# Kernel tuning notes

Measured on AMD Instinct MI355X. Metric: run time of the kernel, lower is better.

Reference implementation:

```python
import jax, jax.numpy as jnp
import numpy as np

Vx, Vy, B, N, C, H, M_VIEWS = 8, 8, 4, 196, 768, 12, 4
DH = C // H
SCALE = DH ** -0.5
HID = 4 * C


def _layer_norm(x, w, b, eps=1e-5):
    mu = jnp.mean(x, axis=-1, keepdims=True)
    var = jnp.mean((x - mu) ** 2, axis=-1, keepdims=True)
    return (x - mu) / jnp.sqrt(var + eps) * w + b


def setup_inputs() -> dict:
    key = jax.random.key(0)
    ks = jax.random.split(key, 32)
    s = 0.02
    inp = {
        "xs": jax.random.normal(ks[0], (Vx, B, N, C), jnp.float32),
        "ys": jax.random.normal(ks[1], (Vy, B, N, C), jnp.float32),
        "xposes": jax.random.randint(ks[2], (Vx, B, N, 2), 0, N),
        "yposes": jax.random.randint(ks[3], (Vy, B, N, 2), 0, N),
        "rel_ids": jax.random.randint(ks[4], (Vx * M_VIEWS,), 0, Vy),
        "M": M_VIEWS,
        # self-attention params (qkv_bias=False, proj has bias)
        "qkv_w": jax.random.normal(ks[5], (3 * C, C), jnp.float32) * s,
        "attn_proj_w": jax.random.normal(ks[6], (C, C), jnp.float32) * s,
        "attn_proj_b": jnp.zeros((C,), jnp.float32),
        # cross-attention params
        "q_w": jax.random.normal(ks[7], (C, C), jnp.float32) * s,
        "k_w": jax.random.normal(ks[8], (C, C), jnp.float32) * s,
        "v_w": jax.random.normal(ks[9], (C, C), jnp.float32) * s,
        "cross_proj_w": jax.random.normal(ks[10], (C, C), jnp.float32) * s,
        "cross_proj_b": jnp.zeros((C,), jnp.float32),
        # MLP
        "fc1_w": jax.random.normal(ks[11], (HID, C), jnp.float32) * s,
        "fc1_b": jnp.zeros((HID,), jnp.float32),
        "fc2_w": jax.random.normal(ks[12], (C, HID), jnp.float32) * s,
        "fc2_b": jnp.zeros((C,), jnp.float32),
        # layer norms
        "ln1_w": jnp.ones((C,), jnp.float32), "ln1_b": jnp.zeros((C,), jnp.float32),
        "ln2_w": jnp.ones((C,), jnp.float32), "ln2_b": jnp.zeros((C,), jnp.float32),
        "ln3_w": jnp.ones((C,), jnp.float32), "ln3_b": jnp.zeros((C,), jnp.float32),
        "lny_w": jnp.ones((C,), jnp.float32), "lny_b": jnp.zeros((C,), jnp.float32),
    }
    return inp


def _forward(xs, ys, rel_ids, M,
             qkv_w, attn_proj_w, attn_proj_b,
             q_w, k_w, v_w, cross_proj_w, cross_proj_b,
             fc1_w, fc1_b, fc2_w, fc2_b,
             ln1_w, ln1_b, ln2_w, ln2_b, ln3_w, ln3_b, lny_w, lny_b):
    vx, b, nx, c = xs.shape
    vy, _, ny, _ = ys.shape
    x = xs.reshape(vx * b, nx, c)

    # ---- self-attention over each target view (rope=None) ----
    h = _layer_norm(x, ln1_w, ln1_b)
    qkv = (h @ qkv_w.T).reshape(vx * b, nx, 3, H, DH)
    q = jnp.transpose(qkv[:, :, 0], (0, 2, 1, 3))  # (VB,H,N,dh)
    k = jnp.transpose(qkv[:, :, 1], (0, 2, 1, 3))
    v = jnp.transpose(qkv[:, :, 2], (0, 2, 1, 3))
    attn = jax.nn.softmax(jnp.einsum('bhnd,bhkd->bhnk', q, k) * SCALE, axis=-1)
    o = jnp.einsum('bhnk,bhkd->bnhd', attn, v).reshape(vx * b, nx, c)
    x = x + (o @ attn_proj_w.T + attn_proj_b)

    # ---- batched multi-view cross-attention ----
    xn = _layer_norm(x.reshape(vx, b, nx, c), ln2_w, ln2_b)
    yn = _layer_norm(ys, lny_w, lny_b)
    qs = (xn @ q_w.T).reshape(vx, b, nx, H, DH)
    ks = (yn @ k_w.T).reshape(vy, b, ny, H, DH)
    vs = (yn @ v_w.T).reshape(vy, b, ny, H, DH)
    ks_r = ks[rel_ids].reshape(vx, M, b, ny, H, DH)  # index_select + group
    vs_r = vs[rel_ids].reshape(vx, M, b, ny, H, DH)
    # q is broadcast across the M group dim (no materialized expand)
    scores = jnp.einsum('vbnhd,vmbkhd->vmbhnk', qs, ks_r) * SCALE
    a = jax.nn.softmax(scores, axis=-1)
    o = jnp.einsum('vmbhnk,vmbkhd->vmbnhd', a, vs_r).reshape(vx, M, b, nx, c)
    o = o @ cross_proj_w.T + cross_proj_b  # (Vx,M,B,Nx,C)
    merged = jnp.max(o, axis=1).reshape(vx * b, nx, c)  # max-merge over M
    x = x + merged

    # ---- MLP ----
    h = _layer_norm(x, ln3_w, ln3_b)
    x = x + (jax.nn.gelu(h @ fc1_w.T + fc1_b, approximate=False) @ fc2_w.T + fc2_b)
    return x.reshape(vx, b, nx, c)


def reference(xs, ys, xposes, yposes, rel_ids, M,
              qkv_w, attn_proj_w, attn_proj_b,
              q_w, k_w, v_w, cross_proj_w, cross_proj_b,
              fc1_w, fc1_b, fc2_w, fc2_b,
              ln1_w, ln1_b, ln2_w, ln2_b, ln3_w, ln3_b, lny_w, lny_b):
    # xposes/yposes unused because rope=None in this configuration
    return _forward(xs, ys, rel_ids, M,
                    qkv_w, attn_proj_w, attn_proj_b,
                    q_w, k_w, v_w, cross_proj_w, cross_proj_b,
                    fc1_w, fc1_b, fc2_w, fc2_b,
                    ln1_w, ln1_b, ln2_w, ln2_b, ln3_w, ln3_b, lny_w, lny_b)
```

## Files before the change

kernel.cpp:

```cpp
#include <hip/hip_runtime.h>
#include <hip/hip_bf16.h>
#include <stdint.h>
#include <math.h>

#define H_ 12
#define NQ 196
#define CD 768
#define HIDD 3072
#define VX 8
#define VY 8
#define BB 4
#define MV 4
#define VBB 32
#define ROWS 6272
#define CROSS_ROWS 25088
#define SCALE_LOG2E 0.180336880260608f

typedef __attribute__((ext_vector_type(8))) short short8;
typedef __attribute__((ext_vector_type(4))) float f32x4;
typedef __attribute__((ext_vector_type(4))) unsigned short u16x4;
typedef unsigned short u16;

#define AS1 __attribute__((address_space(1)))
#define AS3 __attribute__((address_space(3)))

__device__ __forceinline__ float bf2f(u16 u){
  union { unsigned int i; float f; } v; v.i = ((unsigned int)u) << 16; return v.f;
}
__device__ __forceinline__ u16 f2bf(float f){
  union { unsigned int i; float f; } v; v.f = f;
  return (u16)((v.i + 0x7fff + ((v.i >> 16) & 1)) >> 16);
}
__device__ __forceinline__ unsigned int f2u(float f){
  union { unsigned int i; float f; } v; v.f = f; return v.i;
}

struct CastSegs {
  const float* src[8];
  u16* dst[8];
  int cum[9];
};
__global__ __launch_bounds__(256) void k_cast_all(CastSegs segs){
  int i = blockIdx.x * 256 + threadIdx.x;
  if (i >= segs.cum[8]) return;
  int s = 0;
  #pragma unroll
  for (int k = 1; k < 8; k++) s += (i >= segs.cum[k]);
  const int off = i - segs.cum[s];
  segs.dst[s][off] = f2bf(segs.src[s][off]);
}

__device__ __forceinline__ void ln_row(const float* __restrict__ x,
    const float* __restrict__ w, const float* __restrict__ b,
    u16* __restrict__ out, int row, int tid){
  const float* xr = x + (size_t)row * CD;
  float v0 = xr[tid], v1 = xr[tid + 256], v2 = xr[tid + 512];
  float s  = v0 + v1 + v2;
  float s2 = v0*v0 + v1*v1 + v2*v2;
  __shared__ float red[8];
  const int lane = tid & 63, wid = tid >> 6;
  #pragma unroll
  for (int o = 32; o; o >>= 1){ s += __shfl_down(s, o); s2 += __shfl_down(s2, o); }
  if (lane == 0){ red[wid] = s; red[wid + 4] = s2; }
  __syncthreads();
  if (tid == 0){
    red[0] = red[0] + red[1] + red[2] + red[3];
    red[4] = red[4] + red[5] + red[6] + red[7];
  }
  __syncthreads();
  const float mu   = red[0] * (1.f/768.f);
  const float var  = red[4] * (1.f/768.f) - mu*mu;
  const float rstd = rsqrtf(var + 1e-5f);
  u16* orow = out + (size_t)row * CD;
  orow[tid]       = f2bf((v0 - mu)*rstd*w[tid]       + b[tid]);
  orow[tid + 256] = f2bf((v1 - mu)*rstd*w[tid + 256] + b[tid + 256]);
  orow[tid + 512] = f2bf((v2 - mu)*rstd*w[tid + 512] + b[tid + 512]);
}

__global__ __launch_bounds__(256) void k_ln_bf16(const float* __restrict__ x,
    const float* __restrict__ w, const float* __restrict__ b, u16* __restrict__ out){
  ln_row(x, w, b, out, blockIdx.x, threadIdx.x);
}

__global__ __launch_bounds__(256) void k_ln_bf16x2(
    const float* __restrict__ x0, const float* __restrict__ w0,
    const float* __restrict__ b0, u16* __restrict__ o0,
    const float* __restrict__ x1, const float* __restrict__ w1,
    const float* __restrict__ b1, u16* __restrict__ o1){
  const int bid = blockIdx.x;
  if (bid < ROWS) ln_row(x0, w0, b0, o0, bid, threadIdx.x);
  else            ln_row(x1, w1, b1, o1, bid - ROWS, threadIdx.x);
}

template<int EPI, int TM>
__global__ __launch_bounds__(256) void k_gemm_bt(
    const u16* __restrict__ A, const u16* __restrict__ B,
    float* __restrict__ Cf, u16* __restrict__ Cb,
    const float* __restrict__ bias, const float* __restrict__ resid,
    int M, int N, int K){
  __shared__ u16 As[TM * 64];
  __shared__ u16 Bs[128 * 64];
  const int tid  = threadIdx.x;
  const int lane = tid & 63;
  const int wave = tid >> 6;
  const int wr = wave >> 1, wc = wave & 1;

  const int gx = gridDim.x;
  const int nwg = gx * gridDim.y;
  const int orig = blockIdx.y * gx + blockIdx.x;
  const int q8 = nwg >> 3, r8 = nwg & 7;
  const int xcd = orig & 7, bse = orig >> 3;
  const int wg = (xcd < r8 ? xcd * (q8 + 1) : r8 * (q8 + 1) + (xcd - r8) * q8) + bse;
  const int m0 = (wg / gx) * TM, n0 = (wg % gx) * 128;

  constexpr int MF = TM / 64;
  f32x4 acc[TM/32][4];
  #pragma unroll
  for (int i = 0; i < TM/32; i++)
    #pragma unroll
    for (int j = 0; j < 4; j++) acc[i][j] = (f32x4){0.f, 0.f, 0.f, 0.f};
  (void)MF;

  const int lrow = lane >> 3;
  const int lcol = ((lane & 7) ^ lrow) * 8;
  const u16* arow = A + (size_t)(m0 + wave*(TM/4) + lrow) * K + lcol;
  const u16* brow = B + (size_t)(n0 + wave*32 + lrow) * K + lcol;

  for (int k0 = 0; k0 < K; k0 += 64){
    #pragma unroll
    for (int i = 0; i < TM/32; i++)
      __builtin_amdgcn_global_load_lds(
        (const AS1 void*)(arow + (size_t)i*8*K + k0),
        (AS3 void*)(As + (wave*(TM/4) + i*8)*64), 16, 0, 0);
    #pragma unroll
    for (int i = 0; i < 4; i++)
      __builtin_amdgcn_global_load_lds(
        (const AS1 void*)(brow + (size_t)i*8*K + k0),
        (AS3 void*)(Bs + (wave*32 + i*8)*64), 16, 0, 0);
    __syncthreads();
    const u16* ab = As + (wr*(TM/2) + (lane & 15))*64;
    const u16* bb = Bs + (wc*64 + (lane & 15))*64;
    const int r7 = lane & 7;
    #pragma unroll
    for (int kk = 0; kk < 2; kk++){
      const int sl = (((lane >> 4) + 4*kk) ^ r7) * 8;
      short8 af[TM/32], bfr[4];
      #pragma unroll
      for (int f = 0; f < TM/32; f++) af[f] = *(const short8*)(ab + f*1024 + sl);
      #pragma unroll
      for (int f = 0; f < 4; f++)     bfr[f] = *(const short8*)(bb + f*1024 + sl);
      #pragma unroll
      for (int i = 0; i < TM/32; i++)
        #pragma unroll
        for (int j = 0; j < 4; j++)
          acc[i][j] = __builtin_amdgcn_mfma_f32_16x16x32_bf16(af[i], bfr[j], acc[i][j], 0, 0, 0);
    }
    __syncthreads();
  }

  #pragma unroll
  for (int i = 0; i < TM/32; i++){
    const int rb = m0 + wr*(TM/2) + i*16 + (lane >> 4)*4;
    #pragma unroll
    for (int j = 0; j < 4; j++){
      const int col = n0 + wc*64 + j*16 + (lane & 15);
      #pragma unroll
      for (int r = 0; r < 4; r++){
        const size_t idx = (size_t)(rb + r) * N + col;
        const float v = acc[i][j][r];
        if (EPI == 0){
          Cb[idx] = f2bf(v);
        } else if (EPI == 1){
          Cf[idx] = v + bias[col] + resid[idx];
        } else if (EPI == 2){
          Cf[idx] = v + bias[col];
        } else if (EPI == 3){
          float g = v + bias[col];
          g = 0.5f * g * (1.f + erff(g * 0.70710678118654752f));
          Cb[idx] = f2bf(g);
        } else {
          Cb[idx] = f2bf(v + bias[col]);
        }
      }
    }
  }
}

template<int MODE>
__global__ __launch_bounds__(256) void k_attn_mfma(
    const u16* __restrict__ Qb, const u16* __restrict__ Kb, const u16* __restrict__ Vb,
    u16* __restrict__ Ob, const int* __restrict__ rel_ids){
  __shared__ u16 Kl[2][2048];
  __shared__ u16 Vl[2][2048];

  size_t qbase, kbase, vbase, obase;
  int qstr, kstr;
  if (MODE == 0){
    const int vb = blockIdx.x / H_, h = blockIdx.x % H_;
    qbase = (size_t)vb * NQ * 2304 + h * 64; qstr = 2304;
    kbase = qbase + 768; vbase = qbase + 1536; kstr = 2304;
    obase = (size_t)vb * NQ * CD + h * 64;
  } else {
    const int h = blockIdx.x % H_; int t = blockIdx.x / H_;
    const int b = t % BB; t /= BB;
    const int m = t % MV; const int vx = t / MV;
    const int rel = rel_ids[vx * MV + m];
    qbase = ((size_t)(vx * BB + b) * NQ) * CD + h * 64; qstr = CD;
    kbase = ((size_t)(rel * BB + b) * NQ) * 1536 + h * 64; kstr = 1536;
    vbase = kbase + 768;
    obase = ((size_t)((vx * MV + m) * BB + b) * NQ) * CD + h * 64;
  }

  const int tid  = threadIdx.x;
  const int lane = tid & 63;
  const int wave = tid >> 6;
  const int lq   = lane & 15;
  const int g    = lane >> 4;

  short8 qfrag[4][2];
  #pragma unroll
  for (int qf = 0; qf < 4; qf++){
    int qrow = wave*64 + qf*16 + lq; if (qrow > 195) qrow = 195;
    const u16* qp = Qb + qbase + (size_t)qrow * qstr + g*8;
    qfrag[qf][0] = *(const short8*)(qp);
    qfrag[qf][1] = *(const short8*)(qp + 32);
  }

  f32x4 oacc[4][4];
  #pragma unroll
  for (int i = 0; i < 4; i++)
    #pragma unroll
    for (int j = 0; j < 4; j++) oacc[i][j] = (f32x4){0.f,0.f,0.f,0.f};
  float l_[4] = {0.f, 0.f, 0.f, 0.f};

  const int skey  = tid >> 3;
  const int sslot = (tid & 7) ^ (skey & 7);
  const int vkey = lane >> 1;
  const int vdh  = wave*16 + (lane & 1)*8;

  auto STAGE = [&](int nb, int t0n){
    int kg = t0n + skey; if (kg > 195) kg = 195;
    __builtin_amdgcn_global_load_lds(
        (const AS1 void*)(Kb + kbase + (size_t)kg*kstr + sslot*8),
        (AS3 void*)(&Kl[nb][wave*512]), 16, 0, 0);
    int vg = t0n + vkey; if (vg > 195) vg = 195;
    __builtin_amdgcn_global_load_lds(
        (const AS1 void*)(Vb + vbase + (size_t)vg*kstr + vdh),
        (AS3 void*)(&Vl[nb][wave*512]), 16, 0, 0);
  };

  union U8 { unsigned u[4]; short8 s; };

  STAGE(0, 0);
  __syncthreads();

  for (int t = 0; t < 7; t++){
    const int cb = t & 1;
    const int t0 = t * 32;
    if (t < 6) STAGE(cb ^ 1, t0 + 32);

    f32x4 sacc[4][2];
    #pragma unroll
    for (int qf = 0; qf < 4; qf++)
      #pragma unroll
      for (int kf = 0; kf < 2; kf++) sacc[qf][kf] = (f32x4){0.f,0.f,0.f,0.f};
    __builtin_amdgcn_s_setprio(1);
    #pragma unroll
    for (int kf = 0; kf < 2; kf++){
      const int key = kf*16 + lq;
      #pragma unroll
      for (int ks = 0; ks < 2; ks++){
        short8 kfrag = *(const short8*)(&Kl[cb][key*64 + (((ks<<2) + g) ^ (key & 7))*8]);
        #pragma unroll
        for (int qf = 0; qf < 4; qf++)
          sacc[qf][kf] = __builtin_amdgcn_mfma_f32_16x16x32_bf16(kfrag, qfrag[qf][ks], sacc[qf][kf], 0, 0, 0);
      }
    }
    __builtin_amdgcn_s_setprio(0);

    const AS3 u16* vp = (const AS3 u16*)(&Vl[cb][0]) + (size_t)lane*4;
    uint2 tr0a, tr0b, tr1a, tr1b, tr2a, tr2b, tr3a, tr3b;
    asm volatile("ds_read_b64_tr_b16 %0, %1 offset:0"    : "=&v"(tr0a) : "v"(vp));
    asm volatile("ds_read_b64_tr_b16 %0, %1 offset:512"  : "=&v"(tr0b) : "v"(vp));
    asm volatile("ds_read_b64_tr_b16 %0, %1 offset:1024" : "=&v"(tr1a) : "v"(vp));
    asm volatile("ds_read_b64_tr_b16 %0, %1 offset:1536" : "=&v"(tr1b) : "v"(vp));
    asm volatile("ds_read_b64_tr_b16 %0, %1 offset:2048" : "=&v"(tr2a) : "v"(vp));
    asm volatile("ds_read_b64_tr_b16 %0, %1 offset:2560" : "=&v"(tr2b) : "v"(vp));
    asm volatile("ds_read_b64_tr_b16 %0, %1 offset:3072" : "=&v"(tr3a) : "v"(vp));
    asm volatile("ds_read_b64_tr_b16 %0, %1 offset:3584" : "=&v"(tr3b) : "v"(vp));

    short8 vfrag[4];
    #pragma unroll
    for (int qf = 0; qf < 4; qf++){
      float p[8], ps = 0.f;
      #pragma unroll
      for (int kf = 0; kf < 2; kf++)
        #pragma unroll
        for (int r = 0; r < 4; r++){
          const int key = t0 + kf*16 + g*4 + r;
          const float e = exp2f(sacc[qf][kf][r] * SCALE_LOG2E);
          p[kf*4 + r] = (key < 196) ? e : 0.f;
          ps += p[kf*4 + r];
        }
      ps += __shfl_xor(ps, 16);
      ps += __shfl_xor(ps, 32);
      l_[qf] += ps;
      U8 pk;
      pk.u[0] = (f2u(p[0]) >> 16) | (f2u(p[1]) & 0xffff0000u);
      pk.u[1] = (f2u(p[2]) >> 16) | (f2u(p[3]) & 0xffff0000u);
      pk.u[2] = (f2u(p[4]) >> 16) | (f2u(p[5]) & 0xffff0000u);
      pk.u[3] = (f2u(p[6]) >> 16) | (f2u(p[7]) & 0xffff0000u);

      if (qf == 0){
        asm volatile("s_waitcnt lgkmcnt(0)" ::: "memory");
        __builtin_amdgcn_sched_barrier(0);
        U8 v0; v0.u[0]=tr0a.x; v0.u[1]=tr0a.y; v0.u[2]=tr0b.x; v0.u[3]=tr0b.y; vfrag[0]=v0.s;
        U8 v1; v1.u[0]=tr1a.x; v1.u[1]=tr1a.y; v1.u[2]=tr1b.x; v1.u[3]=tr1b.y; vfrag[1]=v1.s;
        U8 v2; v2.u[0]=tr2a.x; v2.u[1]=tr2a.y; v2.u[2]=tr2b.x; v2.u[3]=tr2b.y; vfrag[2]=v2.s;
        U8 v3; v3.u[0]=tr3a.x; v3.u[1]=tr3a.y; v3.u[2]=tr3b.x; v3.u[3]=tr3b.y; vfrag[3]=v3.s;
      }
      __builtin_amdgcn_s_setprio(1);
      #pragma unroll
      for (int dhf = 0; dhf < 4; dhf++)
        oacc[qf][dhf] = __builtin_amdgcn_mfma_f32_16x16x32_bf16(vfrag[dhf], pk.s, oacc[qf][dhf], 0, 0, 0);
      __builtin_amdgcn_s_setprio(0);
    }
    __syncthreads();
  }

  #pragma unroll
  for (int qf = 0; qf < 4; qf++){
    const int qrow = wave*64 + qf*16 + lq;
    if (qrow < 196){
      const float inv = 1.f / l_[qf];
      u16* orow = Ob + obase + (size_t)qrow * CD;
      #pragma unroll
      for (int dhf = 0; dhf < 4; dhf++){
        uint2 pk;
        pk.x = (unsigned)f2bf(oacc[qf][dhf][0]*inv) | ((unsigned)f2bf(oacc[qf][dhf][1]*inv) << 16);
        pk.y = (unsigned)f2bf(oacc[qf][dhf][2]*inv) | ((unsigned)f2bf(oacc[qf][dhf][3]*inv) << 16);
        *(uint2*)(orow + dhf*16 + g*4) = pk;
      }
    }
  }
}

__global__ __launch_bounds__(256) void k_maxmerge(const u16* __restrict__ op,
                                                  float* __restrict__ x){
  const int idx = blockIdx.x * 256 + threadIdx.x;
  const int n4 = VX * BB * NQ * CD / 4;
  if (idx >= n4) return;
  const int inner = idx % (NQ * CD / 4);
  const int vb = idx / (NQ * CD / 4);
  const int vx = vb >> 2, b = vb & 3;
  const size_t ms = (size_t)BB * NQ * CD / 4;
  const size_t base = ((size_t)vx * MV * BB + b) * (NQ * CD / 4) + inner;
  const u16x4* op4 = (const u16x4*)op;
  u16x4 a0 = op4[base], a1 = op4[base + ms], a2 = op4[base + 2*ms], a3 = op4[base + 3*ms];
  float* xo = x + (size_t)idx * 4;
  #pragma unroll
  for (int j = 0; j < 4; j++){
    float v = fmaxf(fmaxf(bf2f(a0[j]), bf2f(a1[j])), fmaxf(bf2f(a2[j]), bf2f(a3[j])));
    xo[j] += v;
  }
}

extern "C" void kernel_launch(void* const* d_in, const int* in_sizes, int n_in,
                              void* d_out, int out_size, void* d_ws, size_t ws_size,
                              hipStream_t stream){
  const float* xs           = (const float*)d_in[0];
  const float* ys           = (const float*)d_in[1];
  const int*   rel_ids      = (const int*)  d_in[4];
  const float* qkv_w        = (const float*)d_in[6];
  const float* attn_proj_w  = (const float*)d_in[7];
  const float* attn_proj_b  = (const float*)d_in[8];
  const float* q_w          = (const float*)d_in[9];
  const float* k_w          = (const float*)d_in[10];
  const float* v_w          = (const float*)d_in[11];
  const float* cross_proj_w = (const float*)d_in[12];
  const float* cross_proj_b = (const float*)d_in[13];
  const float* fc1_w        = (const float*)d_in[14];
  const float* fc1_b        = (const float*)d_in[15];
  const float* fc2_w        = (const float*)d_in[16];
  const float* fc2_b        = (const float*)d_in[17];
  const float* ln1_w        = (const float*)d_in[18];
  const float* ln1_b        = (const float*)d_in[19];
  const float* ln2_w        = (const float*)d_in[20];
  const float* ln2_b        = (const float*)d_in[21];
  const float* ln3_w        = (const float*)d_in[22];
  const float* ln3_b        = (const float*)d_in[23];
  const float* lny_w        = (const float*)d_in[24];
  const float* lny_b        = (const float*)d_in[25];
  float* out = (float*)d_out;

  char* ws = (char*)d_ws;
  size_t off = 0;
  auto alloc = [&](size_t bytes) -> char* {
    char* p = ws + off; off += (bytes + 255) & ~(size_t)255; return p;
  };
  u16* wb_qkv   = (u16*)alloc((size_t)2304*768*2);
  u16* wb_aproj = (u16*)alloc((size_t)768*768*2);
  u16* wb_q     = (u16*)alloc((size_t)768*768*2);
  u16* wb_kv    = (u16*)alloc((size_t)1536*768*2);
  u16* wb_cproj = (u16*)alloc((size_t)768*768*2);
  u16* wb_fc1   = (u16*)alloc((size_t)3072*768*2);
  u16* wb_fc2   = (u16*)alloc((size_t)768*3072*2);
  float* x_ws   = (float*)alloc((size_t)ROWS*CD*4);
  u16* hbuf     = (u16*)alloc((size_t)ROWS*CD*2);
  u16* ynbuf    = (u16*)alloc((size_t)ROWS*CD*2);
  u16* o_self   = (u16*)alloc((size_t)ROWS*CD*2);
  u16* qs       = (u16*)alloc((size_t)ROWS*CD*2);
  u16* kvs      = (u16*)alloc((size_t)ROWS*1536*2);
  u16* o_cross  = (u16*)alloc((size_t)CROSS_ROWS*CD*2);
  char* un = alloc((size_t)CROSS_ROWS*CD*2);
  u16* qkvbuf = (u16*)un;
  u16* oproj  = (u16*)un;
  u16* mid    = (u16*)un;

  CastSegs segs;
  const float* srcs[8] = {qkv_w, attn_proj_w, q_w, k_w, v_w, cross_proj_w, fc1_w, fc2_w};
  u16* dsts[8] = {wb_qkv, wb_aproj, wb_q, wb_kv, wb_kv + 768*768, wb_cproj, wb_fc1, wb_fc2};
  int lens[8]  = {2304*768, 768*768, 768*768, 768*768, 768*768, 768*768, 3072*768, 3072*768};
  segs.cum[0] = 0;
  for (int i = 0; i < 8; i++){ segs.src[i] = srcs[i]; segs.dst[i] = dsts[i];
                               segs.cum[i+1] = segs.cum[i] + lens[i]; }
  k_cast_all<<<(segs.cum[8] + 255) / 256, 256, 0, stream>>>(segs);

  k_ln_bf16<<<ROWS, 256, 0, stream>>>(xs, ln1_w, ln1_b, hbuf);
  k_gemm_bt<0,128><<<dim3(2304/128, ROWS/128), 256, 0, stream>>>(
      hbuf, wb_qkv, nullptr, qkvbuf, nullptr, nullptr, ROWS, 2304, 768);
  k_attn_mfma<0><<<VBB * H_, 256, 0, stream>>>(qkvbuf, qkvbuf, qkvbuf, o_self, rel_ids);
  k_gemm_bt<1,64><<<dim3(768/128, ROWS/64), 256, 0, stream>>>(
      o_self, wb_aproj, x_ws, nullptr, attn_proj_b, xs, ROWS, 768, 768);

  k_ln_bf16x2<<<2*ROWS, 256, 0, stream>>>(x_ws, ln2_w, ln2_b, hbuf,
                                          ys, lny_w, lny_b, ynbuf);
  k_gemm_bt<0,64><<<dim3(768/128, ROWS/64), 256, 0, stream>>>(
      hbuf, wb_q, nullptr, qs, nullptr, nullptr, ROWS, 768, 768);
  k_gemm_bt<0,128><<<dim3(1536/128, ROWS/128), 256, 0, stream>>>(
      ynbuf, wb_kv, nullptr, kvs, nullptr, nullptr, ROWS, 1536, 768);
  k_attn_mfma<1><<<VX * MV * BB * H_, 256, 0, stream>>>(qs, kvs, kvs, o_cross, rel_ids);
  k_gemm_bt<4,128><<<dim3(768/128, CROSS_ROWS/128), 256, 0, stream>>>(
      o_cross, wb_cproj, nullptr, oproj, cross_proj_b, nullptr, CROSS_ROWS, 768, 768);
  k_maxmerge<<<(ROWS * CD / 4 + 255) / 256, 256, 0, stream>>>(oproj, x_ws);

  k_ln_bf16<<<ROWS, 256, 0, stream>>>(x_ws, ln3_w, ln3_b, hbuf);
  k_gemm_bt<3,128><<<dim3(HIDD/128, ROWS/128), 256, 0, stream>>>(
      hbuf, wb_fc1, nullptr, mid, fc1_b, nullptr, ROWS, HIDD, 768);
  k_gemm_bt<1,64><<<dim3(768/128, ROWS/64), 256, 0, stream>>>(
      mid, wb_fc2, out, nullptr, fc2_b, x_ws, ROWS, 768, HIDD);
}
```

Before: 385.3 us.

## Double-buffer small-tile GEMMs, fuse max-merge with LN3, skip padded attention rows

Adds an optional double-buffered LDS path to the bf16 GEMM. The next K-tile is staged while the current one is computed, with one barrier per iteration instead of two, and it is enabled for the TM=64 GEMMs. The separate max-merge kernel and the LN3 kernel are fused into one row kernel that reads the four views, updates the residual and normalizes in one pass, removing a read and write of the residual. The attention kernel skips MFMA and softmax work for query fragments beyond the 196 valid rows. Double buffering doubles LDS use, which may reduce occupancy.

```diff
diff --git a/kernel.cpp b/kernel.cpp
--- a/kernel.cpp
+++ b/kernel.cpp
@@ -92,14 +92,58 @@
   else            ln_row(x1, w1, b1, o1, bid - ROWS, threadIdx.x);
 }
 
-template<int EPI, int TM>
+__global__ __launch_bounds__(256) void k_mmln(const u16* __restrict__ op,
+    float* __restrict__ x, const float* __restrict__ w, const float* __restrict__ b,
+    u16* __restrict__ out){
+  const int row = blockIdx.x, tid = threadIdx.x;
+  const int n = row % NQ, vb = row / NQ;
+  const int vx = vb >> 2, bb = vb & 3;
+  const size_t r0 = ((size_t)(vx * MV) * BB + bb) * NQ + n;
+  const size_t ms = (size_t)BB * NQ;
+  float* xr = x + (size_t)row * CD;
+  float v[3], s = 0.f, s2 = 0.f;
+  #pragma unroll
+  for (int j = 0; j < 3; j++){
+    const int col = tid + j*256;
+    float mx =        bf2f(op[(r0       ) * CD + col]);
+    mx = fmaxf(mx,    bf2f(op[(r0 +   ms) * CD + col]));
+    mx = fmaxf(mx,    bf2f(op[(r0 + 2*ms) * CD + col]));
+    mx = fmaxf(mx,    bf2f(op[(r0 + 3*ms) * CD + col]));
+    const float val = xr[col] + mx;
+    xr[col] = val;
+    v[j] = val;
+    s += val; s2 += val*val;
+  }
+  __shared__ float red[8];
+  const int lane = tid & 63, wid = tid >> 6;
+  #pragma unroll
+  for (int o = 32; o; o >>= 1){ s += __shfl_down(s, o); s2 += __shfl_down(s2, o); }
+  if (lane == 0){ red[wid] = s; red[wid + 4] = s2; }
+  __syncthreads();
+  if (tid == 0){
+    red[0] = red[0] + red[1] + red[2] + red[3];
+    red[4] = red[4] + red[5] + red[6] + red[7];
+  }
+  __syncthreads();
+  const float mu   = red[0] * (1.f/768.f);
+  const float var  = red[4] * (1.f/768.f) - mu*mu;
+  const float rstd = rsqrtf(var + 1e-5f);
+  u16* orow = out + (size_t)row * CD;
+  #pragma unroll
+  for (int j = 0; j < 3; j++){
+    const int col = tid + j*256;
+    orow[col] = f2bf((v[j] - mu)*rstd*w[col] + b[col]);
+  }
+}
+
+template<int EPI, int TM, int DB>
 __global__ __launch_bounds__(256) void k_gemm_bt(
     const u16* __restrict__ A, const u16* __restrict__ B,
     float* __restrict__ Cf, u16* __restrict__ Cb,
     const float* __restrict__ bias, const float* __restrict__ resid,
     int M, int N, int K){
-  __shared__ u16 As[TM * 64];
-  __shared__ u16 Bs[128 * 64];
+  __shared__ u16 As[(DB + 1) * TM * 64];
+  __shared__ u16 Bs[(DB + 1) * 128 * 64];
   const int tid  = threadIdx.x;
   const int lane = tid & 63;
   const int wave = tid >> 6;
@@ -113,33 +157,33 @@
   const int wg = (xcd < r8 ? xcd * (q8 + 1) : r8 * (q8 + 1) + (xcd - r8) * q8) + bse;
   const int m0 = (wg / gx) * TM, n0 = (wg % gx) * 128;
 
-  constexpr int MF = TM / 64;
   f32x4 acc[TM/32][4];
   #pragma unroll
   for (int i = 0; i < TM/32; i++)
     #pragma unroll
     for (int j = 0; j < 4; j++) acc[i][j] = (f32x4){0.f, 0.f, 0.f, 0.f};
-  (void)MF;
 
   const int lrow = lane >> 3;
   const int lcol = ((lane & 7) ^ lrow) * 8;
   const u16* arow = A + (size_t)(m0 + wave*(TM/4) + lrow) * K + lcol;
   const u16* brow = B + (size_t)(n0 + wave*32 + lrow) * K + lcol;
 
-  for (int k0 = 0; k0 < K; k0 += 64){
+  auto STG = [&](int nb, int k0){
     #pragma unroll
     for (int i = 0; i < TM/32; i++)
       __builtin_amdgcn_global_load_lds(
         (const AS1 void*)(arow + (size_t)i*8*K + k0),
-        (AS3 void*)(As + (wave*(TM/4) + i*8)*64), 16, 0, 0);
+        (AS3 void*)(As + nb*TM*64 + (wave*(TM/4) + i*8)*64), 16, 0, 0);
     #pragma unroll
     for (int i = 0; i < 4; i++)
       __builtin_amdgcn_global_load_lds(
         (const AS1 void*)(brow + (size_t)i*8*K + k0),
-        (AS3 void*)(Bs + (wave*32 + i*8)*64), 16, 0, 0);
-    __syncthreads();
-    const u16* ab = As + (wr*(TM/2) + (lane & 15))*64;
-    const u16* bb = Bs + (wc*64 + (lane & 15))*64;
+        (AS3 void*)(Bs + nb*128*64 + (wave*32 + i*8)*64), 16, 0, 0);
+  };
+
+  auto COMPUTE = [&](int nb){
+    const u16* ab = As + nb*TM*64 + (wr*(TM/2) + (lane & 15))*64;
+    const u16* bb = Bs + nb*128*64 + (wc*64 + (lane & 15))*64;
     const int r7 = lane & 7;
     #pragma unroll
     for (int kk = 0; kk < 2; kk++){
@@ -155,7 +199,25 @@
         for (int j = 0; j < 4; j++)
           acc[i][j] = __builtin_amdgcn_mfma_f32_16x16x32_bf16(af[i], bfr[j], acc[i][j], 0, 0, 0);
     }
+  };
+
+  if (DB){
+    const int NT = K >> 6;
+    STG(0, 0);
     __syncthreads();
+    for (int it = 0; it < NT; ++it){
+      const int cb = it & 1;
+      if (it + 1 < NT) STG(cb ^ 1, (it + 1) * 64);
+      COMPUTE(cb);
+      __syncthreads();
+    }
+  } else {
+    for (int k0 = 0; k0 < K; k0 += 64){
+      STG(0, k0);
+      __syncthreads();
+      COMPUTE(0);
+      __syncthreads();
+    }
   }
 
   #pragma unroll
@@ -273,7 +335,8 @@
         short8 kfrag = *(const short8*)(&Kl[cb][key*64 + (((ks<<2) + g) ^ (key & 7))*8]);
         #pragma unroll
         for (int qf = 0; qf < 4; qf++)
-          sacc[qf][kf] = __builtin_amdgcn_mfma_f32_16x16x32_bf16(kfrag, qfrag[qf][ks], sacc[qf][kf], 0, 0, 0);
+          if (wave*64 + qf*16 < NQ)
+            sacc[qf][kf] = __builtin_amdgcn_mfma_f32_16x16x32_bf16(kfrag, qfrag[qf][ks], sacc[qf][kf], 0, 0, 0);
       }
     }
     __builtin_amdgcn_s_setprio(0);
@@ -292,6 +355,7 @@
     short8 vfrag[4];
     #pragma unroll
     for (int qf = 0; qf < 4; qf++){
+      if (wave*64 + qf*16 >= NQ) continue;
       float p[8], ps = 0.f;
       #pragma unroll
       for (int kf = 0; kf < 2; kf++)
@@ -342,26 +406,6 @@
         *(uint2*)(orow + dhf*16 + g*4) = pk;
       }
     }
-  }
-}
-
-__global__ __launch_bounds__(256) void k_maxmerge(const u16* __restrict__ op,
-                                                  float* __restrict__ x){
-  const int idx = blockIdx.x * 256 + threadIdx.x;
-  const int n4 = VX * BB * NQ * CD / 4;
-  if (idx >= n4) return;
-  const int inner = idx % (NQ * CD / 4);
-  const int vb = idx / (NQ * CD / 4);
-  const int vx = vb >> 2, b = vb & 3;
-  const size_t ms = (size_t)BB * NQ * CD / 4;
-  const size_t base = ((size_t)vx * MV * BB + b) * (NQ * CD / 4) + inner;
-  const u16x4* op4 = (const u16x4*)op;
-  u16x4 a0 = op4[base], a1 = op4[base + ms], a2 = op4[base + 2*ms], a3 = op4[base + 3*ms];
-  float* xo = x + (size_t)idx * 4;
-  #pragma unroll
-  for (int j = 0; j < 4; j++){
-    float v = fmaxf(fmaxf(bf2f(a0[j]), bf2f(a1[j])), fmaxf(bf2f(a2[j]), bf2f(a3[j])));
-    xo[j] += v;
   }
 }
 
@@ -427,26 +471,25 @@
   k_cast_all<<<(segs.cum[8] + 255) / 256, 256, 0, stream>>>(segs);
 
   k_ln_bf16<<<ROWS, 256, 0, stream>>>(xs, ln1_w, ln1_b, hbuf);
-  k_gemm_bt<0,128><<<dim3(2304/128, ROWS/128), 256, 0, stream>>>(
+  k_gemm_bt<0,128,0><<<dim3(2304/128, ROWS/128), 256, 0, stream>>>(
       hbuf, wb_qkv, nullptr, qkvbuf, nullptr, nullptr, ROWS, 2304, 768);
   k_attn_mfma<0><<<VBB * H_, 256, 0, stream>>>(qkvbuf, qkvbuf, qkvbuf, o_self, rel_ids);
-  k_gemm_bt<1,64><<<dim3(768/128, ROWS/64), 256, 0, stream>>>(
+  k_gemm_bt<1,64,1><<<dim3(768/128, ROWS/64), 256, 0, stream>>>(
       o_self, wb_aproj, x_ws, nullptr, attn_proj_b, xs, ROWS, 768, 768);
 
   k_ln_bf16x2<<<2*ROWS, 256, 0, stream>>>(x_ws, ln2_w, ln2_b, hbuf,
                                           ys, lny_w, lny_b, ynbuf);
-  k_gemm_bt<0,64><<<dim3(768/128, ROWS/64), 256, 0, stream>>>(
+  k_gemm_bt<0,64,1><<<dim3(768/128, ROWS/64), 256, 0, stream>>>(
       hbuf, wb_q, nullptr, qs, nullptr, nullptr, ROWS, 768, 768);
-  k_gemm_bt<0,128><<<dim3(1536/128, ROWS/128), 256, 0, stream>>>(
+  k_gemm_bt<0,128,0><<<dim3(1536/128, ROWS/128), 256, 0, stream>>>(
       ynbuf, wb_kv, nullptr, kvs, nullptr, nullptr, ROWS, 1536, 768);
   k_attn_mfma<1><<<VX * MV * BB * H_, 256, 0, stream>>>(qs, kvs, kvs, o_cross, rel_ids);
-  k_gemm_bt<4,128><<<dim3(768/128, CROSS_ROWS/128), 256, 0, stream>>>(
+  k_gemm_bt<4,128,0><<<dim3(768/128, CROSS_ROWS/128), 256, 0, stream>>>(
       o_cross, wb_cproj, nullptr, oproj, cross_proj_b, nullptr, CROSS_ROWS, 768, 768);
-  k_maxmerge<<<(ROWS * CD / 4 + 255) / 256, 256, 0, stream>>>(oproj, x_ws);
-
-  k_ln_bf16<<<ROWS, 256, 0, stream>>>(x_ws, ln3_w, ln3_b, hbuf);
-  k_gemm_bt<3,128><<<dim3(HIDD/128, ROWS/128), 256, 0, stream>>>(
+  k_mmln<<<ROWS, 256, 0, stream>>>(oproj, x_ws, ln3_w, ln3_b, hbuf);
+
+  k_gemm_bt<3,128,0><<<dim3(HIDD/128, ROWS/128), 256, 0, stream>>>(
       hbuf, wb_fc1, nullptr, mid, fc1_b, nullptr, ROWS, HIDD, 768);
-  k_gemm_bt<1,64><<<dim3(768/128, ROWS/64), 256, 0, stream>>>(
+  k_gemm_bt<1,64,1><<<dim3(768/128, ROWS/64), 256, 0, stream>>>(
       mid, wb_fc2, out, nullptr, fc2_b, x_ws, ROWS, 768, HIDD);
 }
```

Result: no change. 380.9 us (-1.1%).
